# Kernel tuning notes

Hardware: AMD Instinct MI355X
Metric: run time of the kernel (lower is better)

Reference implementation:

```python
import jax, jax.numpy as jnp
import numpy as np

D_MODEL = 1024
N_HEADS = 16
D_K = D_MODEL // N_HEADS
THETA = 10000.0
B, S = 2, 2048


def _rope(x):
    # x: [B, H, S, Dh], interleaved-pair RoPE with positions arange(S)
    Dh = x.shape[-1]
    inv_freq = 1.0 / (THETA ** (jnp.arange(0, Dh, 2, dtype=jnp.float32) / Dh))  # [Dh/2]
    pos = jnp.arange(x.shape[-2], dtype=jnp.float32)
    ang = pos[:, None] * inv_freq[None, :]                      # [S, Dh/2]
    cos = jnp.repeat(jnp.cos(ang), 2, axis=-1).astype(x.dtype)  # [S, Dh]
    sin = jnp.repeat(jnp.sin(ang), 2, axis=-1).astype(x.dtype)
    # rotate pairs: (x_2k, x_2k+1) -> (-x_2k+1, x_2k)
    xp = x.reshape(*x.shape[:-1], Dh // 2, 2)
    rot = jnp.stack((-xp[..., 1], xp[..., 0]), axis=-1).reshape(x.shape)
    return x * cos + rot * sin


def setup_inputs() -> dict:
    key = jax.random.key(0)
    ks = jax.random.split(key, 5)
    std = (2.0 / (D_MODEL + D_MODEL)) ** 0.5
    return {
        "x": jax.random.normal(ks[0], (B, S, D_MODEL), dtype=jnp.float32),
        "wq": jax.random.normal(ks[1], (D_MODEL, D_MODEL), dtype=jnp.float32) * std,
        "wk": jax.random.normal(ks[2], (D_MODEL, D_MODEL), dtype=jnp.float32) * std,
        "wv": jax.random.normal(ks[3], (D_MODEL, D_MODEL), dtype=jnp.float32) * std,
        "wo": jax.random.normal(ks[4], (D_MODEL, D_MODEL), dtype=jnp.float32) * std,
    }


def reference(x, wq, wk, wv, wo):
    b, s, _ = x.shape
    def split_heads(t):
        return t.reshape(b, s, N_HEADS, D_K).transpose(0, 2, 1, 3)  # [B,H,S,Dk]
    # Linear: y = x @ W.T  (weights stored [out, in])
    q = split_heads(jnp.einsum('bsd,od->bso', x, wq))
    k = split_heads(jnp.einsum('bsd,od->bso', x, wk))
    v = split_heads(jnp.einsum('bsd,od->bso', x, wv))
    q = _rope(q)
    k = _rope(k)
    scores = jnp.einsum('bhqd,bhkd->bhqk', q, k) / jnp.sqrt(jnp.asarray(D_K, x.dtype))
    causal = jnp.tril(jnp.ones((s, s), dtype=bool))
    scores = jnp.where(causal[None, None], scores, -jnp.inf)
    attn = jax.nn.softmax(scores, axis=-1)
    out = jnp.einsum('bhqk,bhkd->bhqd', attn, v)
    out = out.transpose(0, 2, 1, 3).reshape(b, s, D_MODEL)
    return jnp.einsum('bsd,od->bso', out, wo)
```

## Files before the change

kernel.cpp:

```cpp
#include <hip/hip_runtime.h>


typedef unsigned short u16;
typedef __attribute__((ext_vector_type(8))) short short8;
typedef __attribute__((ext_vector_type(4))) float float4v;

typedef const __attribute__((address_space(1))) void GV;
typedef __attribute__((address_space(3))) void LV;

#define VSTR 72
#define QSCL 0.18033688011112042f

__device__ __forceinline__ u16 f2b(float f) {
    union { float f; unsigned int i; } t; t.f = f;
    unsigned int r = t.i + 0x7fffu + ((t.i >> 16) & 1u);
    return (u16)(r >> 16);
}

__global__ __launch_bounds__(256) void cvt_all(
    const float4* __restrict__ x,  const float4* __restrict__ wq,
    const float4* __restrict__ wk, const float4* __restrict__ wv,
    const float4* __restrict__ wo,
    u16* __restrict__ xb, u16* __restrict__ wcat, u16* __restrict__ wob,
    float2* __restrict__ tab)
{
    const int blk = blockIdx.x;
    if (blk >= 4096) {
        const int i = (blk - 4096) * 256 + threadIdx.x;
        const int pos = i >> 5, fi = i & 31;
        const float freq = exp2f((float)fi * -0.4152410118609203f);
        float sn, cs; sincosf((float)pos * freq, &sn, &cs);
        tab[i] = make_float2(cs, sn);
        return;
    }
    const int i = blk * 256 + threadIdx.x;
    const float4* s; u16* d; int off;
    if (i < 524288) { s = x; d = xb; off = i; }
    else {
        const int widx = i - 524288;
        const int w = widx >> 17, o = widx & 131071;
        switch (w) {
            case 0:  s = wq; d = wcat;              break;
            case 1:  s = wk; d = wcat + (1 << 20);  break;
            case 2:  s = wv; d = wcat + (2 << 20);  break;
            default: s = wo; d = wob;               break;
        }
        off = o;
    }
    float4 a = s[2 * off], b = s[2 * off + 1];
    u16 t[8] = {f2b(a.x), f2b(a.y), f2b(a.z), f2b(a.w),
                f2b(b.x), f2b(b.y), f2b(b.z), f2b(b.w)};
    reinterpret_cast<int4*>(d)[off] = *reinterpret_cast<int4*>(t);
}

__global__ __launch_bounds__(512) void gemm_qkv(
    const u16* __restrict__ X, const u16* __restrict__ Wb,
    u16* __restrict__ Yq, u16* __restrict__ Yk, u16* __restrict__ Yv,
    const float2* __restrict__ tab)
{
    __shared__ u16 As[2][256 * 64];
    __shared__ u16 Bs[2][192 * 64];

    const int tid  = threadIdx.x;
    const int wave = tid >> 6;
    const int lane = tid & 63;
    const int quad = lane >> 4;
    const int l16  = lane & 15;
    const int wm = (wave >> 2) * 128;
    const int wn = (wave & 3) * 48;
    const int g = blockIdx.x;
    const int rr = g >> 3;
    const int m0 = ((g & 7) * 2 + (rr >> 4)) * 256;
    const int n0 = (rr & 15) * 192;
    const int lrow = lane >> 3;
    const int cg8  = (lane & 7) ^ lrow;

    float4v acc[8][3];
#pragma unroll
    for (int mt = 0; mt < 8; mt++)
#pragma unroll
        for (int nt = 0; nt < 3; nt++) acc[mt][nt] = (float4v){0.f, 0.f, 0.f, 0.f};

    auto stage = [&](int bsel, int kb) {
#pragma unroll
        for (int t = 0; t < 4; t++) {
            const int I = wave * 4 + t;
            const u16* gp = X + (size_t)(m0 + I * 8 + lrow) * 1024 + kb + cg8 * 8;
            __builtin_amdgcn_global_load_lds((GV*)gp, (LV*)&As[bsel][I * 512], 16, 0, 0);
        }
#pragma unroll
        for (int t = 0; t < 3; t++) {
            const int I = wave * 3 + t;
            const u16* gp = Wb + (size_t)(n0 + I * 8 + lrow) * 1024 + kb + cg8 * 8;
            __builtin_amdgcn_global_load_lds((GV*)gp, (LV*)&Bs[bsel][I * 512], 16, 0, 0);
        }
    };

    stage(0, 0);
    stage(1, 64);

    for (int kbi = 0; kbi < 16; kbi++) {
        const int cur = kbi & 1;
        if (kbi < 15) { asm volatile("s_waitcnt vmcnt(7)" ::: "memory"); }
        else          { asm volatile("s_waitcnt vmcnt(0)" ::: "memory"); }
        __builtin_amdgcn_sched_barrier(0);
        __builtin_amdgcn_s_barrier();
        __builtin_amdgcn_sched_barrier(0);
        __builtin_amdgcn_s_setprio(1);
#pragma unroll
        for (int ks = 0; ks < 2; ks++) {
            const int su = ((ks * 4 + quad) ^ (l16 & 7)) * 8;
            short8 af[8], bf[3];
#pragma unroll
            for (int t = 0; t < 8; t++)
                af[t] = *reinterpret_cast<const short8*>(&As[cur][(wm + t * 16 + l16) * 64 + su]);
#pragma unroll
            for (int t = 0; t < 3; t++)
                bf[t] = *reinterpret_cast<const short8*>(&Bs[cur][(wn + t * 16 + l16) * 64 + su]);
#pragma unroll
            for (int mt = 0; mt < 8; mt++)
#pragma unroll
                for (int nt = 0; nt < 3; nt++)
                    acc[mt][nt] = __builtin_amdgcn_mfma_f32_16x16x32_bf16(af[mt], bf[nt], acc[mt][nt], 0, 0, 0);
        }
        __builtin_amdgcn_s_setprio(0);
        __builtin_amdgcn_sched_barrier(0);
        __builtin_amdgcn_s_barrier();
        __builtin_amdgcn_sched_barrier(0);
        if (kbi < 14) stage(cur, (kbi + 2) * 64);
    }

#pragma unroll
    for (int nt = 0; nt < 3; nt++) {
        const int cg = n0 + wn + nt * 16 + l16;
        const int buf = cg >> 10;
        const int c = cg & 1023;
        u16* dst = (buf == 0) ? Yq : ((buf == 1) ? Yk : Yv);
        const bool rp = (buf < 2);
        const float scl = (buf == 0) ? QSCL : 1.0f;
        const int fi = (cg & 63) >> 1;
#pragma unroll
        for (int mt = 0; mt < 8; mt++)
#pragma unroll
            for (int r = 0; r < 4; r++) {
                const int row = m0 + wm + mt * 16 + quad * 4 + r;
                float v = acc[mt][nt][r];
                if (rp) {
                    const float2 t = tab[((row & 2047) << 5) + fi];
                    const float partner = __shfl_xor(v, 1);
                    v = (l16 & 1) ? fmaf(v, t.x,  partner * t.y)
                                  : fmaf(v, t.x, -partner * t.y);
                }
                dst[(size_t)row * 1024 + c] = f2b(v * scl);
            }
    }
}

__global__ __launch_bounds__(512) void gemm_proj(
    const u16* __restrict__ X, const u16* __restrict__ Wb,
    float* __restrict__ Yf)
{
    __shared__ u16 As[2][256 * 64];
    __shared__ u16 Bs[2][64 * 64];

    const int tid  = threadIdx.x;
    const int wave = tid >> 6;
    const int lane = tid & 63;
    const int quad = lane >> 4;
    const int l16  = lane & 15;
    const int wm = (wave >> 1) * 64;
    const int wn = (wave & 1) * 32;
    const int g = blockIdx.x;
    const int rr = g >> 3;
    const int m0 = ((g & 7) * 2 + (rr >> 4)) * 256;
    const int n0 = (rr & 15) * 64;
    const int lrow = lane >> 3;
    const int cg8  = (lane & 7) ^ lrow;

    float4v acc[4][2];
#pragma unroll
    for (int mt = 0; mt < 4; mt++)
#pragma unroll
        for (int nt = 0; nt < 2; nt++) acc[mt][nt] = (float4v){0.f, 0.f, 0.f, 0.f};

    auto stage = [&](int bsel, int kb) {
#pragma unroll
        for (int t = 0; t < 4; t++) {
            const int I = wave * 4 + t;
            const u16* gp = X + (size_t)(m0 + I * 8 + lrow) * 1024 + kb + cg8 * 8;
            __builtin_amdgcn_global_load_lds((GV*)gp, (LV*)&As[bsel][I * 512], 16, 0, 0);
        }
        {
            const u16* gp = Wb + (size_t)(n0 + wave * 8 + lrow) * 1024 + kb + cg8 * 8;
            __builtin_amdgcn_global_load_lds((GV*)gp, (LV*)&Bs[bsel][wave * 512], 16, 0, 0);
        }
    };

    stage(0, 0);
    stage(1, 64);

    for (int kbi = 0; kbi < 16; kbi++) {
        const int cur = kbi & 1;
        if (kbi < 15) { asm volatile("s_waitcnt vmcnt(5)" ::: "memory"); }
        else          { asm volatile("s_waitcnt vmcnt(0)" ::: "memory"); }
        __builtin_amdgcn_sched_barrier(0);
        __builtin_amdgcn_s_barrier();
        __builtin_amdgcn_sched_barrier(0);
        __builtin_amdgcn_s_setprio(1);
#pragma unroll
        for (int ks = 0; ks < 2; ks++) {
            const int su = ((ks * 4 + quad) ^ (l16 & 7)) * 8;
            short8 af[4], bf[2];
#pragma unroll
            for (int t = 0; t < 4; t++)
                af[t] = *reinterpret_cast<const short8*>(&As[cur][(wm + t * 16 + l16) * 64 + su]);
#pragma unroll
            for (int t = 0; t < 2; t++)
                bf[t] = *reinterpret_cast<const short8*>(&Bs[cur][(wn + t * 16 + l16) * 64 + su]);
#pragma unroll
            for (int mt = 0; mt < 4; mt++)
#pragma unroll
                for (int nt = 0; nt < 2; nt++)
                    acc[mt][nt] = __builtin_amdgcn_mfma_f32_16x16x32_bf16(af[mt], bf[nt], acc[mt][nt], 0, 0, 0);
        }
        __builtin_amdgcn_s_setprio(0);
        __builtin_amdgcn_sched_barrier(0);
        __builtin_amdgcn_s_barrier();
        __builtin_amdgcn_sched_barrier(0);
        if (kbi < 14) stage(cur, (kbi + 2) * 64);
    }

#pragma unroll
    for (int nt = 0; nt < 2; nt++) {
        const int col = n0 + wn + nt * 16 + l16;
#pragma unroll
        for (int mt = 0; mt < 4; mt++)
#pragma unroll
            for (int r = 0; r < 4; r++) {
                const int row = m0 + wm + mt * 16 + quad * 4 + r;
                Yf[(size_t)row * 1024 + col] = acc[mt][nt][r];
            }
    }
}

__global__ __launch_bounds__(256, 2) void attn_kernel(
    const u16* Q, const u16* __restrict__ K,
    const u16* __restrict__ V, u16* O)
{
    __shared__ __align__(16) u16 Vt[2][64 * VSTR];

    const int tid  = threadIdx.x;
    const int wave = tid >> 6;
    const int lane = tid & 63;
    const int quad = lane >> 4;
    const int l16  = lane & 15;
    const int g = blockIdx.x;
    const int xcd = g & 7, slot = g >> 3;
    const int G = (slot >> 4) * 8 + xcd;
    const int qtA = slot & 15;
    const int qtB = 31 - qtA;
    const int b = G & 1, h = G >> 1;
    const size_t base = ((size_t)b * 2048) * 1024 + (size_t)h * 64;

    short8 qfA[2], qfB[2];
    {
        const size_t ra = base + (size_t)(qtA * 64 + wave * 16 + l16) * 1024;
        qfA[0] = *reinterpret_cast<const short8*>(Q + ra + quad * 8);
        qfA[1] = *reinterpret_cast<const short8*>(Q + ra + 32 + quad * 8);
        const size_t rb = base + (size_t)(qtB * 64 + wave * 16 + l16) * 1024;
        qfB[0] = *reinterpret_cast<const short8*>(Q + rb + quad * 8);
        qfB[1] = *reinterpret_cast<const short8*>(Q + rb + 32 + quad * 8);
    }

    float4v oA[4], oB[4];
#pragma unroll
    for (int i = 0; i < 4; i++) { oA[i] = (float4v){0.f,0.f,0.f,0.f}; oB[i] = (float4v){0.f,0.f,0.f,0.f}; }
    float sA = 0.f, sB = 0.f;

    const int srow = tid >> 2;
    const int cb   = (tid & 3) << 4;
    const int sxw  = srow ^ cb;

    const u16* Vp = V + base + (size_t)srow * 1024 + cb;
    const u16* kbase = K + base + (size_t)l16 * 1024 + quad * 8;
    int4 vr0 = *reinterpret_cast<const int4*>(Vp);
    int4 vr1 = *reinterpret_cast<const int4*>(Vp + 8);
    short8 kn[4][2], kc[4][2], vf[4][2];
#pragma unroll
    for (int nt = 0; nt < 4; nt++)
#pragma unroll
        for (int ks = 0; ks < 2; ks++)
            kn[nt][ks] = *reinterpret_cast<const short8*>(kbase + (size_t)(nt * 16) * 1024 + ks * 32);

    {
        const u16* a = reinterpret_cast<const u16*>(&vr0);
        const u16* c = reinterpret_cast<const u16*>(&vr1);
#pragma unroll
        for (int e = 0; e < 8; e++) Vt[0][(cb + e) * VSTR + sxw] = a[e];
#pragma unroll
        for (int e = 0; e < 8; e++) Vt[0][(cb + 8 + e) * VSTR + sxw] = c[e];
    }
    vr0 = *reinterpret_cast<const int4*>(Vp + 65536);
    vr1 = *reinterpret_cast<const int4*>(Vp + 65536 + 8);

    const int qloc = wave * 16 + l16;

    auto qk = [&](const short8 (&qf)[2], float4v (&sacc)[4]) {
#pragma unroll
        for (int nt = 0; nt < 4; nt++) {
            sacc[nt] = (float4v){0.f, 0.f, 0.f, 0.f};
#pragma unroll
            for (int ks = 0; ks < 2; ks++)
                sacc[nt] = __builtin_amdgcn_mfma_f32_16x16x32_bf16(kc[nt][ks], qf[ks], sacc[nt], 0, 0, 0);
        }
    };
    auto smx = [&](const float4v (&sacc)[4], float &sr, short8 (&pa)[2], bool diag) {
        unsigned int w[4][2];
#pragma unroll
        for (int nt = 0; nt < 4; nt++) {
            float p[4];
#pragma unroll
            for (int r = 0; r < 4; r++) {
                float sv = sacc[nt][r];
                if (diag && (nt * 16 + quad * 4 + r > qloc)) sv = -1e30f;
                p[r] = exp2f(sv);
                sr += p[r];
            }
            asm("v_cvt_pk_bf16_f32 %0, %1, %2" : "=v"(w[nt][0]) : "v"(p[0]), "v"(p[1]));
            asm("v_cvt_pk_bf16_f32 %0, %1, %2" : "=v"(w[nt][1]) : "v"(p[2]), "v"(p[3]));
        }
        union { unsigned int u[4]; short8 s8; } t;
        t.u[0] = w[0][0]; t.u[1] = w[0][1]; t.u[2] = w[1][0]; t.u[3] = w[1][1];
        pa[0] = t.s8;
        t.u[0] = w[2][0]; t.u[1] = w[2][1]; t.u[2] = w[3][0]; t.u[3] = w[3][1];
        pa[1] = t.s8;
    };
    auto pv = [&](const short8 (&pa)[2], float4v (&oc)[4]) {
#pragma unroll
        for (int ks = 0; ks < 2; ks++)
#pragma unroll
            for (int dt = 0; dt < 4; dt++)
                oc[dt] = __builtin_amdgcn_mfma_f32_16x16x32_bf16(pa[ks], vf[dt][ks], oc[dt], 0, 0, 0);
    };

    for (int j = 0; j <= qtB; j++) {
        __syncthreads();
        if (j < qtB) {
            u16* D = Vt[(j + 1) & 1];
            const u16* a = reinterpret_cast<const u16*>(&vr0);
            const u16* c = reinterpret_cast<const u16*>(&vr1);
#pragma unroll
            for (int e = 0; e < 8; e++) D[(cb + e) * VSTR + sxw] = a[e];
#pragma unroll
            for (int e = 0; e < 8; e++) D[(cb + 8 + e) * VSTR + sxw] = c[e];
        }
#pragma unroll
        for (int nt = 0; nt < 4; nt++)
#pragma unroll
            for (int ks = 0; ks < 2; ks++) kc[nt][ks] = kn[nt][ks];
        if (j < qtB) {
            if (j + 2 <= qtB) {
                vr0 = *reinterpret_cast<const int4*>(Vp + (size_t)(j + 2) * 65536);
                vr1 = *reinterpret_cast<const int4*>(Vp + (size_t)(j + 2) * 65536 + 8);
            }
            const u16* kb2 = kbase + (size_t)(j + 1) * 65536;
#pragma unroll
            for (int nt = 0; nt < 4; nt++)
#pragma unroll
                for (int ks = 0; ks < 2; ks++)
                    kn[nt][ks] = *reinterpret_cast<const short8*>(kb2 + (size_t)(nt * 16) * 1024 + ks * 32);
        }
        {
            const u16* B = Vt[j & 1];
#pragma unroll
            for (int dt = 0; dt < 4; dt++) {
                const int rb = (dt * 16 + l16) * VSTR;
#pragma unroll
                for (int ks = 0; ks < 2; ks++) {
                    const int k1 = (ks * 32 + quad * 4) ^ (dt << 4);
                    const int k2 = (ks * 32 + 16 + quad * 4) ^ (dt << 4);
                    union { struct { uint2 lo, hi; } p; short8 s8; } u;
                    u.p.lo = *reinterpret_cast<const uint2*>(&B[rb + k1]);
                    u.p.hi = *reinterpret_cast<const uint2*>(&B[rb + k2]);
                    vf[dt][ks] = u.s8;
                }
            }
        }

        if (j <= qtA) {
            float4v xA[4], xB[4];
            qk(qfA, xA);
            qk(qfB, xB);
            short8 paA[2], paB[2];
            smx(xA, sA, paA, j == qtA);
            smx(xB, sB, paB, false);
            pv(paA, oA);
            pv(paB, oB);
        } else {
            float4v xB[4];
            qk(qfB, xB);
            short8 paB[2];
            smx(xB, sB, paB, j == qtB);
            pv(paB, oB);
        }
    }

    float tA = sA, tB = sB;
    tA += __shfl_xor(tA, 16); tA += __shfl_xor(tA, 32);
    tB += __shfl_xor(tB, 16); tB += __shfl_xor(tB, 32);
#pragma unroll
    for (int r = 0; r < 4; r++) {
        const int rl = quad * 4 + r;
        const float invA = 1.0f / __shfl(tA, rl);
        const float invB = 1.0f / __shfl(tB, rl);
        const size_t rowA = base + (size_t)(qtA * 64 + wave * 16 + rl) * 1024;
        const size_t rowB = base + (size_t)(qtB * 64 + wave * 16 + rl) * 1024;
#pragma unroll
        for (int dt = 0; dt < 4; dt++) {
            O[rowA + dt * 16 + l16] = f2b(oA[dt][r] * invA);
            O[rowB + dt * 16 + l16] = f2b(oB[dt][r] * invB);
        }
    }
}

extern "C" void kernel_launch(void* const* d_in, const int* in_sizes, int n_in,
                              void* d_out, int out_size, void* d_ws, size_t ws_size,
                              hipStream_t stream) {
    (void)in_sizes; (void)n_in; (void)out_size; (void)ws_size;
    const float* x  = (const float*)d_in[0];
    const float* wq = (const float*)d_in[1];
    const float* wk = (const float*)d_in[2];
    const float* wv = (const float*)d_in[3];
    const float* wo = (const float*)d_in[4];

    const size_t MN = (size_t)4096 * 1024;

    u16* xb   = (u16*)d_out;
    u16* wcat = xb + MN;
    float2* tab = (float2*)(wcat + (size_t)3072 * 1024);
    u16* qbuf = (u16*)d_ws;
    u16* kbuf = qbuf + MN;
    u16* vbuf = kbuf + MN;
    u16* wob  = vbuf + MN;

    cvt_all<<<4352, 256, 0, stream>>>((const float4*)x, (const float4*)wq,
                                      (const float4*)wk, (const float4*)wv,
                                      (const float4*)wo, xb, wcat, wob, tab);
    gemm_qkv<<<256, 512, 0, stream>>>(xb, wcat, qbuf, kbuf, vbuf, tab);
    attn_kernel<<<512, 256, 0, stream>>>(qbuf, kbuf, vbuf, qbuf);
    gemm_proj<<<256, 512, 0, stream>>>(qbuf, wob, (float*)d_out);
}
```

Measured before the change: 213.6 us.

## Widen attention KV tile to 128 keys with restructured V staging and K prefetch

The causal attention loop now processes 128 keys per iteration instead of 64. This halves the number of block barriers and double-buffer swaps, and each LDS V tile is reused across twice as many keys. V staging now uses 2 threads per row with 4 int4 loads, and K for the next tile is loaded mid-iteration after QK instead of through a separate kn register copy. The cost is higher register pressure (8x2 K fragments, 8 score accumulators) and a larger LDS footprint, which could reduce occupancy at 2 blocks per SM. The diagonal tile now masks at 64-key granularity within 128, so about half a tile of extra work is done on the diagonal.

```diff
diff --git a/kernel.cpp b/kernel.cpp
--- a/kernel.cpp
+++ b/kernel.cpp
@@ -8,7 +8,7 @@
 typedef const __attribute__((address_space(1))) void GV;
 typedef __attribute__((address_space(3))) void LV;
 
-#define VSTR 72
+#define VSTR 136
 #define QSCL 0.18033688011112042f
 
 __device__ __forceinline__ u16 f2b(float f) {
@@ -259,6 +259,8 @@
     const int G = (slot >> 4) * 8 + xcd;
     const int qtA = slot & 15;
     const int qtB = 31 - qtA;
+    const int jAmax = qtA >> 1;
+    const int jBmax = qtB >> 1;
     const int b = G & 1, h = G >> 1;
     const size_t base = ((size_t)b * 2048) * 1024 + (size_t)h * 64;
 
@@ -277,131 +279,139 @@
     for (int i = 0; i < 4; i++) { oA[i] = (float4v){0.f,0.f,0.f,0.f}; oB[i] = (float4v){0.f,0.f,0.f,0.f}; }
     float sA = 0.f, sB = 0.f;
 
-    const int srow = tid >> 2;
-    const int cb   = (tid & 3) << 4;
-    const int sxw  = srow ^ cb;
-
-    const u16* Vp = V + base + (size_t)srow * 1024 + cb;
+    const int srow2 = tid >> 1;
+    const int dbase = (tid & 1) << 5;
+    const u16* Vp = V + base + (size_t)srow2 * 1024 + dbase;
     const u16* kbase = K + base + (size_t)l16 * 1024 + quad * 8;
-    int4 vr0 = *reinterpret_cast<const int4*>(Vp);
-    int4 vr1 = *reinterpret_cast<const int4*>(Vp + 8);
-    short8 kn[4][2], kc[4][2], vf[4][2];
-#pragma unroll
-    for (int nt = 0; nt < 4; nt++)
-#pragma unroll
-        for (int ks = 0; ks < 2; ks++)
-            kn[nt][ks] = *reinterpret_cast<const short8*>(kbase + (size_t)(nt * 16) * 1024 + ks * 32);
-
-    {
-        const u16* a = reinterpret_cast<const u16*>(&vr0);
-        const u16* c = reinterpret_cast<const u16*>(&vr1);
-#pragma unroll
-        for (int e = 0; e < 8; e++) Vt[0][(cb + e) * VSTR + sxw] = a[e];
-#pragma unroll
-        for (int e = 0; e < 8; e++) Vt[0][(cb + 8 + e) * VSTR + sxw] = c[e];
-    }
-    vr0 = *reinterpret_cast<const int4*>(Vp + 65536);
-    vr1 = *reinterpret_cast<const int4*>(Vp + 65536 + 8);
-
-    const int qloc = wave * 16 + l16;
-
-    auto qk = [&](const short8 (&qf)[2], float4v (&sacc)[4]) {
-#pragma unroll
-        for (int nt = 0; nt < 4; nt++) {
+
+    int4 vr[4];
+#pragma unroll
+    for (int t = 0; t < 4; t++)
+        vr[t] = *reinterpret_cast<const int4*>(Vp + t * 8);
+
+    short8 kc[8][2];
+    auto loadK = [&](int jn) {
+        const u16* kp = kbase + (size_t)jn * 131072;
+#pragma unroll
+        for (int nt = 0; nt < 8; nt++)
+#pragma unroll
+            for (int kd = 0; kd < 2; kd++)
+                kc[nt][kd] = *reinterpret_cast<const short8*>(kp + (size_t)(nt * 16) * 1024 + kd * 32);
+    };
+    loadK(0);
+
+    auto stageV = [&](u16* D) {
+#pragma unroll
+        for (int t = 0; t < 4; t++) {
+            const int d0 = dbase + 8 * t;
+            const int sxw = srow2 ^ (((d0 >> 4) & 3) << 4);
+            const u16* a = reinterpret_cast<const u16*>(&vr[t]);
+#pragma unroll
+            for (int e = 0; e < 8; e++) D[(d0 + e) * VSTR + sxw] = a[e];
+        }
+    };
+    stageV(Vt[0]);
+#pragma unroll
+    for (int t = 0; t < 4; t++)
+        vr[t] = *reinterpret_cast<const int4*>(Vp + 131072 + t * 8);
+
+    const int qrelA = ((qtA & 1) << 6) + wave * 16 + l16;
+    const int qrelB = ((qtB & 1) << 6) + wave * 16 + l16;
+
+    auto qk8 = [&](const short8 (&qf)[2], float4v (&sacc)[8]) {
+#pragma unroll
+        for (int nt = 0; nt < 8; nt++) {
             sacc[nt] = (float4v){0.f, 0.f, 0.f, 0.f};
 #pragma unroll
-            for (int ks = 0; ks < 2; ks++)
-                sacc[nt] = __builtin_amdgcn_mfma_f32_16x16x32_bf16(kc[nt][ks], qf[ks], sacc[nt], 0, 0, 0);
-        }
-    };
-    auto smx = [&](const float4v (&sacc)[4], float &sr, short8 (&pa)[2], bool diag) {
-        unsigned int w[4][2];
-#pragma unroll
-        for (int nt = 0; nt < 4; nt++) {
+            for (int kd = 0; kd < 2; kd++)
+                sacc[nt] = __builtin_amdgcn_mfma_f32_16x16x32_bf16(kc[nt][kd], qf[kd], sacc[nt], 0, 0, 0);
+        }
+    };
+    auto smx8 = [&](const float4v (&sacc)[8], float &sr, short8 (&pa)[4], bool diag, int qrel) {
+        unsigned int w[8][2];
+#pragma unroll
+        for (int nt = 0; nt < 8; nt++) {
             float p[4];
 #pragma unroll
             for (int r = 0; r < 4; r++) {
                 float sv = sacc[nt][r];
-                if (diag && (nt * 16 + quad * 4 + r > qloc)) sv = -1e30f;
+                if (diag && (nt * 16 + quad * 4 + r > qrel)) sv = -1e30f;
                 p[r] = exp2f(sv);
                 sr += p[r];
             }
             asm("v_cvt_pk_bf16_f32 %0, %1, %2" : "=v"(w[nt][0]) : "v"(p[0]), "v"(p[1]));
             asm("v_cvt_pk_bf16_f32 %0, %1, %2" : "=v"(w[nt][1]) : "v"(p[2]), "v"(p[3]));
         }
-        union { unsigned int u[4]; short8 s8; } t;
-        t.u[0] = w[0][0]; t.u[1] = w[0][1]; t.u[2] = w[1][0]; t.u[3] = w[1][1];
-        pa[0] = t.s8;
-        t.u[0] = w[2][0]; t.u[1] = w[2][1]; t.u[2] = w[3][0]; t.u[3] = w[3][1];
-        pa[1] = t.s8;
-    };
-    auto pv = [&](const short8 (&pa)[2], float4v (&oc)[4]) {
-#pragma unroll
-        for (int ks = 0; ks < 2; ks++)
-#pragma unroll
-            for (int dt = 0; dt < 4; dt++)
-                oc[dt] = __builtin_amdgcn_mfma_f32_16x16x32_bf16(pa[ks], vf[dt][ks], oc[dt], 0, 0, 0);
-    };
-
-    for (int j = 0; j <= qtB; j++) {
+#pragma unroll
+        for (int ks = 0; ks < 4; ks++) {
+            union { unsigned int u[4]; short8 s8; } t;
+            t.u[0] = w[2 * ks][0];     t.u[1] = w[2 * ks][1];
+            t.u[2] = w[2 * ks + 1][0]; t.u[3] = w[2 * ks + 1][1];
+            pa[ks] = t.s8;
+        }
+    };
+
+    for (int j = 0; j <= jBmax; j++) {
         __syncthreads();
-        if (j < qtB) {
-            u16* D = Vt[(j + 1) & 1];
-            const u16* a = reinterpret_cast<const u16*>(&vr0);
-            const u16* c = reinterpret_cast<const u16*>(&vr1);
-#pragma unroll
-            for (int e = 0; e < 8; e++) D[(cb + e) * VSTR + sxw] = a[e];
-#pragma unroll
-            for (int e = 0; e < 8; e++) D[(cb + 8 + e) * VSTR + sxw] = c[e];
-        }
-#pragma unroll
-        for (int nt = 0; nt < 4; nt++)
-#pragma unroll
-            for (int ks = 0; ks < 2; ks++) kc[nt][ks] = kn[nt][ks];
-        if (j < qtB) {
-            if (j + 2 <= qtB) {
-                vr0 = *reinterpret_cast<const int4*>(Vp + (size_t)(j + 2) * 65536);
-                vr1 = *reinterpret_cast<const int4*>(Vp + (size_t)(j + 2) * 65536 + 8);
-            }
-            const u16* kb2 = kbase + (size_t)(j + 1) * 65536;
-#pragma unroll
-            for (int nt = 0; nt < 4; nt++)
-#pragma unroll
-                for (int ks = 0; ks < 2; ks++)
-                    kn[nt][ks] = *reinterpret_cast<const short8*>(kb2 + (size_t)(nt * 16) * 1024 + ks * 32);
-        }
-        {
-            const u16* B = Vt[j & 1];
-#pragma unroll
-            for (int dt = 0; dt < 4; dt++) {
-                const int rb = (dt * 16 + l16) * VSTR;
-#pragma unroll
-                for (int ks = 0; ks < 2; ks++) {
+        if (j < jBmax) stageV(Vt[(j + 1) & 1]);
+        if (j + 2 <= jBmax) {
+#pragma unroll
+            for (int t = 0; t < 4; t++)
+                vr[t] = *reinterpret_cast<const int4*>(Vp + (size_t)(j + 2) * 131072 + t * 8);
+        }
+        const u16* Bt = Vt[j & 1];
+
+        if (j <= jAmax) {
+            float4v xA[8];
+            short8 paA[4], paB[4];
+            qk8(qfA, xA);
+            smx8(xA, sA, paA, j == jAmax, qrelA);
+            float4v xB[8];
+            qk8(qfB, xB);
+            if (j < jBmax) loadK(j + 1);
+            smx8(xB, sB, paB, false, qrelB);
+#pragma unroll
+            for (int ks = 0; ks < 4; ks++) {
+                short8 vfk[4];
+#pragma unroll
+                for (int dt = 0; dt < 4; dt++) {
+                    const int rb = (dt * 16 + l16) * VSTR;
                     const int k1 = (ks * 32 + quad * 4) ^ (dt << 4);
                     const int k2 = (ks * 32 + 16 + quad * 4) ^ (dt << 4);
                     union { struct { uint2 lo, hi; } p; short8 s8; } u;
-                    u.p.lo = *reinterpret_cast<const uint2*>(&B[rb + k1]);
-                    u.p.hi = *reinterpret_cast<const uint2*>(&B[rb + k2]);
-                    vf[dt][ks] = u.s8;
+                    u.p.lo = *reinterpret_cast<const uint2*>(&Bt[rb + k1]);
+                    u.p.hi = *reinterpret_cast<const uint2*>(&Bt[rb + k2]);
+                    vfk[dt] = u.s8;
+                }
+#pragma unroll
+                for (int dt = 0; dt < 4; dt++) {
+                    oA[dt] = __builtin_amdgcn_mfma_f32_16x16x32_bf16(paA[ks], vfk[dt], oA[dt], 0, 0, 0);
+                    oB[dt] = __builtin_amdgcn_mfma_f32_16x16x32_bf16(paB[ks], vfk[dt], oB[dt], 0, 0, 0);
                 }
             }
-        }
-
-        if (j <= qtA) {
-            float4v xA[4], xB[4];
-            qk(qfA, xA);
-            qk(qfB, xB);
-            short8 paA[2], paB[2];
-            smx(xA, sA, paA, j == qtA);
-            smx(xB, sB, paB, false);
-            pv(paA, oA);
-            pv(paB, oB);
         } else {
-            float4v xB[4];
-            qk(qfB, xB);
-            short8 paB[2];
-            smx(xB, sB, paB, j == qtB);
-            pv(paB, oB);
+            float4v xB[8];
+            short8 paB[4];
+            qk8(qfB, xB);
+            if (j < jBmax) loadK(j + 1);
+            smx8(xB, sB, paB, j == jBmax, qrelB);
+#pragma unroll
+            for (int ks = 0; ks < 4; ks++) {
+                short8 vfk[4];
+#pragma unroll
+                for (int dt = 0; dt < 4; dt++) {
+                    const int rb = (dt * 16 + l16) * VSTR;
+                    const int k1 = (ks * 32 + quad * 4) ^ (dt << 4);
+                    const int k2 = (ks * 32 + 16 + quad * 4) ^ (dt << 4);
+                    union { struct { uint2 lo, hi; } p; short8 s8; } u;
+                    u.p.lo = *reinterpret_cast<const uint2*>(&Bt[rb + k1]);
+                    u.p.hi = *reinterpret_cast<const uint2*>(&Bt[rb + k2]);
+                    vfk[dt] = u.s8;
+                }
+#pragma unroll
+                for (int dt = 0; dt < 4; dt++)
+                    oB[dt] = __builtin_amdgcn_mfma_f32_16x16x32_bf16(paB[ks], vfk[dt], oB[dt], 0, 0, 0);
+            }
         }
     }
 
```

After: 313.9 us. 46.9% more time.
